# Kernel tuning notes

Measured on AMD Instinct MI355X. Metric: run time of the kernel, lower is better.

The kernel has to match this reference:

```python
import jax, jax.numpy as jnp
import numpy as np
import itertools

DIM_X, DIM_Y = 3, 3
MAX_DIGIT = DIM_X * DIM_Y          # 9
NUM_NODES = MAX_DIGIT ** 2         # 81
EMBED = 16
HID = 96
BATCH = 256
ITERS = 4


def determine_edges(dim_x, dim_y):
    md = dim_x * dim_y
    rows = []
    for r in range(md):
        for c in range(md):
            s = {(r, i) for i in range(md)} | {(i, c) for i in range(md)}
            xm, ym = r // dim_x * dim_x, c // dim_y * dim_y
            s |= set(itertools.product(range(xm, xm + dim_x), range(ym, ym + dim_y)))
            s -= {(r, c)}
            rows.append(sorted(i * md + j for i, j in s))
    return np.asarray(rows, dtype=np.int32)  # [81, 20]


def mlp3(x, w0, b0, w1, b1, w2, b2):
    # MLP([a,b,c,d]): two ReLU hidden layers, linear output
    x = jax.nn.relu(x @ w0.T + b0)
    x = jax.nn.relu(x @ w1.T + b1)
    return x @ w2.T + b2


def setup_inputs() -> dict:
    key = jax.random.key(0)
    keys = iter(jax.random.split(key, 40))

    def lin(din, dout):
        kw, kb = jax.random.split(next(keys))
        lim = 1.0 / np.sqrt(din)
        w = jax.random.uniform(kw, (dout, din), jnp.float32, -lim, lim)
        b = jax.random.uniform(kb, (dout,), jnp.float32, -lim, lim)
        return w, b

    embed = jax.random.normal(next(keys), (MAX_DIGIT + 1, EMBED), jnp.float32)

    in_w0, in_b0 = lin(EMBED, HID); in_w1, in_b1 = lin(HID, HID); in_w2, in_b2 = lin(HID, HID)
    f_w0, f_b0 = lin(2 * HID, HID); f_w1, f_b1 = lin(HID, HID); f_w2, f_b2 = lin(HID, HID)
    g_w0, g_b0 = lin(2 * HID, HID); g_w1, g_b1 = lin(HID, HID); g_w2, g_b2 = lin(HID, HID)
    r_w0, r_b0 = lin(HID, HID); r_w1, r_b1 = lin(HID, HID); r_w2, r_b2 = lin(HID, MAX_DIGIT)

    lim = 1.0 / np.sqrt(HID)
    lstm_wih = jax.random.uniform(next(keys), (4 * HID, HID), jnp.float32, -lim, lim)
    lstm_whh = jax.random.uniform(next(keys), (4 * HID, HID), jnp.float32, -lim, lim)
    lstm_bih = jax.random.uniform(next(keys), (4 * HID,), jnp.float32, -lim, lim)
    lstm_bhh = jax.random.uniform(next(keys), (4 * HID,), jnp.float32, -lim, lim)

    grids = jax.random.randint(next(keys), (BATCH, NUM_NODES), 0, MAX_DIGIT + 1)
    c0 = jax.random.normal(next(keys), (BATCH * NUM_NODES, HID), jnp.float32)
    edges = jnp.asarray(determine_edges(DIM_X, DIM_Y))

    return dict(embed=embed,
                in_w0=in_w0, in_b0=in_b0, in_w1=in_w1, in_b1=in_b1, in_w2=in_w2, in_b2=in_b2,
                f_w0=f_w0, f_b0=f_b0, f_w1=f_w1, f_b1=f_b1, f_w2=f_w2, f_b2=f_b2,
                g_w0=g_w0, g_b0=g_b0, g_w1=g_w1, g_b1=g_b1, g_w2=g_w2, g_b2=g_b2,
                lstm_wih=lstm_wih, lstm_whh=lstm_whh, lstm_bih=lstm_bih, lstm_bhh=lstm_bhh,
                r_w0=r_w0, r_b0=r_b0, r_w1=r_w1, r_b1=r_b1, r_w2=r_w2, r_b2=r_b2,
                c0=c0, grids=grids, edges=edges, iters=ITERS)


def reference(embed,
              in_w0, in_b0, in_w1, in_b1, in_w2, in_b2,
              f_w0, f_b0, f_w1, f_b1, f_w2, f_b2,
              g_w0, g_b0, g_w1, g_b1, g_w2, g_b2,
              lstm_wih, lstm_whh, lstm_bih, lstm_bhh,
              r_w0, r_b0, r_w1, r_b1, r_w2, r_b2,
              c0, grids, edges, iters):
    B, N = grids.shape
    K = edges.shape[1]
    emb = embed[grids]                                   # [B, N, EMBED]
    X = mlp3(emb, in_w0, in_b0, in_w1, in_b1, in_w2, in_b2)  # [B, N, HID]
    H = X
    h = X.reshape(B * N, HID)
    c = c0
    outputs = []
    for _ in range(iters):
        # gather neighbor states: [B, N, K, HID]
        Hn = H[:, edges]
        Hs = jnp.broadcast_to(H[:, :, None, :], Hn.shape)
        pair = jnp.concatenate([Hs, Hn], axis=-1)        # [B, N, K, 2*HID]
        M = mlp3(pair, f_w0, f_b0, f_w1, f_b1, f_w2, f_b2).sum(axis=2)  # [B, N, HID]
        gin = mlp3(jnp.concatenate([X, M], axis=-1),
                   g_w0, g_b0, g_w1, g_b1, g_w2, g_b2).reshape(B * N, HID)
        # single-step LSTM (torch gate order: i, f, g, o)
        gates = gin @ lstm_wih.T + lstm_bih + h @ lstm_whh.T + lstm_bhh
        gi, gf, gg, go = jnp.split(gates, 4, axis=-1)
        c = jax.nn.sigmoid(gf) * c + jax.nn.sigmoid(gi) * jnp.tanh(gg)
        h = jax.nn.sigmoid(go) * jnp.tanh(c)
        H = h.reshape(B, N, HID)
        outputs.append(mlp3(H, r_w0, r_b0, r_w1, r_b1, r_w2, r_b2))  # [B, N, MAX_DIGIT]
    return jnp.stack(outputs)  # [iters, B, N, MAX_DIGIT]
```

## Files before the change

kernel.cpp:

```cpp
#include <hip/hip_runtime.h>
#include <hip/hip_bf16.h>

typedef __hip_bfloat16 bf16;
typedef __attribute__((ext_vector_type(8))) short short8;
typedef __attribute__((ext_vector_type(8))) __bf16 bf16x8;
typedef __attribute__((ext_vector_type(4))) float f32x4;

#define BN 20736
#define NNODE 81
#define KNB 20

__device__ inline float bf2f(short s) {
  union { unsigned u; float f; } x; x.u = ((unsigned)(unsigned short)s) << 16; return x.f;
}
__device__ inline short f2bf(float f) {
  __hip_bfloat16 h = __float2bfloat16(f);
  return *reinterpret_cast<short*>(&h);
}
__device__ inline bf16x8 ld8(const bf16* p) {
  return __builtin_bit_cast(bf16x8, *(const short8*)p);
}

__device__ inline void zacc3(f32x4 acc[3]) {
  #pragma unroll
  for (int nt = 0; nt < 3; ++nt) acc[nt] = (f32x4){0.f, 0.f, 0.f, 0.f};
}
__device__ inline void load_w48(const bf16* __restrict__ W, int ldw, int n0, int lr, int lq,
                                bf16x8 wf[3][3]) {
  #pragma unroll
  for (int nt = 0; nt < 3; ++nt)
    #pragma unroll
    for (int ks = 0; ks < 3; ++ks)
      wf[nt][ks] = ld8(&W[(size_t)(n0 + nt * 16 + lr) * ldw + ks * 32 + lq * 8]);
}
__device__ inline void gemm48(const bf16x8 af[3], const bf16x8 wf[3][3], f32x4 acc[3]) {
  #pragma unroll
  for (int ks = 0; ks < 3; ++ks)
    #pragma unroll
    for (int nt = 0; nt < 3; ++nt)
      acc[nt] = __builtin_amdgcn_mfma_f32_16x16x32_bf16(af[ks], wf[nt][ks], acc[nt], 0, 0, 0);
}
__device__ inline void acc_store_cs(float* xw, const f32x4 acc[3], int lr, int lq, int n0) {
  #pragma unroll
  for (int nt = 0; nt < 3; ++nt)
    #pragma unroll
    for (int r = 0; r < 4; ++r)
      xw[(lq * 4 + r) * 100 + n0 + nt * 16 + lr] = acc[nt][r];
}
__device__ inline void xbuf_frag(const float* xw, int lr, int lq,
                                 const float* __restrict__ bias, float bscale,
                                 const bf16* residRow, int act,
                                 bf16x8 af[3]) {
  #pragma unroll
  for (int ks = 0; ks < 3; ++ks) {
    const int c0 = ks * 32 + lq * 8;
    float4 x0 = *(const float4*)&xw[lr * 100 + c0];
    float4 x1 = *(const float4*)&xw[lr * 100 + c0 + 4];
    float xv[8] = {x0.x, x0.y, x0.z, x0.w, x1.x, x1.y, x1.z, x1.w};
    if (bias) {
      float4 b0 = *(const float4*)&bias[c0];
      float4 b1 = *(const float4*)&bias[c0 + 4];
      float bv[8] = {b0.x, b0.y, b0.z, b0.w, b1.x, b1.y, b1.z, b1.w};
      #pragma unroll
      for (int j = 0; j < 8; ++j) xv[j] += bscale * bv[j];
    }
    if (residRow) {
      short8 r8 = *(const short8*)&residRow[c0];
      #pragma unroll
      for (int j = 0; j < 8; ++j) xv[j] += bf2f(r8[j]);
    }
    short8 o;
    #pragma unroll
    for (int j = 0; j < 8; ++j) {
      float v = xv[j];
      if (act) v = fmaxf(v, 0.f);
      o[j] = f2bf(v);
    }
    af[ks] = __builtin_bit_cast(bf16x8, o);
  }
}
__device__ inline void store_frag(bf16* dst, int lq, const bf16x8 af[3]) {
  #pragma unroll
  for (int ks = 0; ks < 3; ++ks)
    *(short8*)&dst[ks * 32 + lq * 8] = __builtin_bit_cast(short8, af[ks]);
}

__global__ __launch_bounds__(256) void prep_k(
    const float* in_w1, const float* in_w2, const float* f_w1, const float* f_w2,
    const float* g_w1, const float* g_w2, const float* r_w0, const float* r_w1,
    const float* r_w2, const float* wih, const float* whh, const float* g_w0,
    const float* f_w0, const float* in_w0, const float* f_b0,
    bf16* inw1b, bf16* inw2b, bf16* fw1b, bf16* fw2b,
    bf16* gw1b, bf16* gw2b, bf16* rw0b, bf16* rw1b,
    bf16* rw2b, bf16* wihb, bf16* whhb, bf16* gw0b,
    bf16* wfnb, bf16* w0pb, float* bias_fn)
{
  int idx = blockIdx.x * 256 + threadIdx.x;
  int y = blockIdx.y;
  const float* src = nullptr; bf16* dst = nullptr; int cnt = 0;
  switch (y) {
    case 0:  src = in_w1; dst = inw1b; cnt = 9216;  break;
    case 1:  src = in_w2; dst = inw2b; cnt = 9216;  break;
    case 2:  src = f_w1;  dst = fw1b;  cnt = 9216;  break;
    case 3:  src = f_w2;  dst = fw2b;  cnt = 9216;  break;
    case 4:  src = g_w1;  dst = gw1b;  cnt = 9216;  break;
    case 5:  src = g_w2;  dst = gw2b;  cnt = 9216;  break;
    case 6:  src = r_w0;  dst = rw0b;  cnt = 9216;  break;
    case 7:  src = r_w1;  dst = rw1b;  cnt = 9216;  break;
    case 8:  src = r_w2;  dst = rw2b;  cnt = 864;   break;
    case 9:  src = wih;   dst = wihb;  cnt = 36864; break;
    case 10: src = whh;   dst = whhb;  cnt = 36864; break;
    case 11: src = g_w0;  dst = gw0b;  cnt = 18432; break;
    case 12: {
      if (idx < 18432) {
        int n = idx / 96, k = idx - n * 96;
        float v = (n < 96) ? f_w0[n * 192 + k] : f_w0[(n - 96) * 192 + 96 + k];
        wfnb[idx] = __float2bfloat16(v);
      }
      return;
    }
    case 13: {
      if (idx < 3072) {
        int n = idx >> 5, k = idx & 31;
        w0pb[idx] = __float2bfloat16(k < 16 ? in_w0[n * 16 + k] : 0.f);
      }
      return;
    }
    default: {
      if (idx < 192) bias_fn[idx] = (idx < 96) ? f_b0[idx] : 0.f;
      return;
    }
  }
  if (idx < cnt) dst[idx] = __float2bfloat16(src[idx]);
}

__global__ __launch_bounds__(256) void embed_k(const float* __restrict__ embed,
                                               const int* __restrict__ grids,
                                               bf16* __restrict__ emb) {
  int idx = blockIdx.x * 256 + threadIdx.x;
  if (idx >= BN * 32) return;
  int r = idx >> 5, k = idx & 31;
  emb[idx] = __float2bfloat16(k < 16 ? embed[grids[r] * 16 + k] : 0.f);
}

__global__ __launch_bounds__(256) void fused_in_k(
    const bf16* __restrict__ emb, const bf16* __restrict__ w0pb, const float* __restrict__ in_b0,
    const bf16* __restrict__ inw1b, const float* __restrict__ in_b1,
    const bf16* __restrict__ inw2b, const float* __restrict__ in_b2,
    const bf16* __restrict__ gw0b, const float* __restrict__ g_b0,
    const bf16* __restrict__ wfnb, const float* __restrict__ bias_fn,
    bf16* __restrict__ X, bf16* __restrict__ Xg, bf16* __restrict__ P)
{
  __shared__ float xbuf[2][2][1600];
  const int t = threadIdx.x, w = t >> 6, lane = t & 63, lr = lane & 15, lq = lane >> 4;
  const int mh = w >> 1, ch = w & 1, n0 = ch * 48;
  const int m0 = blockIdx.x * 32 + mh * 16;
  float* x0 = xbuf[0][mh];
  float* x1 = xbuf[1][mh];
  bf16x8 wf[3][3]; f32x4 acc[3]; bf16x8 af[3];

  bf16x8 a0 = ld8(&emb[(size_t)(m0 + lr) * 32 + lq * 8]);
  #pragma unroll
  for (int nt = 0; nt < 3; ++nt)
    wf[nt][0] = ld8(&w0pb[(size_t)(n0 + nt * 16 + lr) * 32 + lq * 8]);
  zacc3(acc);
  #pragma unroll
  for (int nt = 0; nt < 3; ++nt)
    acc[nt] = __builtin_amdgcn_mfma_f32_16x16x32_bf16(a0, wf[nt][0], acc[nt], 0, 0, 0);
  acc_store_cs(x0, acc, lr, lq, n0);
  __syncthreads();
  xbuf_frag(x0, lr, lq, in_b0, 1.f, nullptr, 1, af);
  load_w48(inw1b, 96, n0, lr, lq, wf); zacc3(acc); gemm48(af, wf, acc);
  acc_store_cs(x1, acc, lr, lq, n0);
  __syncthreads();
  xbuf_frag(x1, lr, lq, in_b1, 1.f, nullptr, 1, af);
  load_w48(inw2b, 96, n0, lr, lq, wf); zacc3(acc); gemm48(af, wf, acc);
  acc_store_cs(x0, acc, lr, lq, n0);
  __syncthreads();
  bf16x8 xf[3];
  xbuf_frag(x0, lr, lq, in_b2, 1.f, nullptr, 0, xf);
  if (ch == 0) store_frag(&X[(size_t)(m0 + lr) * 96], lq, xf);
  load_w48(gw0b, 192, n0, lr, lq, wf); zacc3(acc); gemm48(xf, wf, acc);
  acc_store_cs(x1, acc, lr, lq, n0);
  __syncthreads();
  xbuf_frag(x1, lr, lq, g_b0, 1.f, nullptr, 0, af);
  if (ch == 0) store_frag(&Xg[(size_t)(m0 + lr) * 96], lq, af);
  #pragma unroll
  for (int ph = 0; ph < 2; ++ph) {
    float* xb = ph ? x1 : x0;
    load_w48(wfnb + (size_t)ph * 96 * 96, 96, n0, lr, lq, wf); zacc3(acc); gemm48(xf, wf, acc);
    acc_store_cs(xb, acc, lr, lq, n0);
    __syncthreads();
    xbuf_frag(xb, lr, lq, bias_fn + ph * 96, 1.f, nullptr, 0, af);
    if (ch == 0) store_frag(&P[(size_t)(m0 + lr) * 192 + ph * 96], lq, af);
  }
}

__global__ __launch_bounds__(256) void edge_k(
    const bf16* __restrict__ P, const bf16* __restrict__ w1bf,
    const float* __restrict__ b1, const int* __restrict__ edges,
    const bf16* __restrict__ fw2b, const float* __restrict__ f_b2,
    bf16* __restrict__ M)
{
  __shared__ short zs[160 * 104];
  __shared__ short sbuf[16 * 104];
  const int t = threadIdx.x;
  const int swz = (blockIdx.x & 7) * 324 + (blockIdx.x >> 3);
  const int ng0 = swz * 2;
  const int w = t >> 6, lane = t & 63, lr = lane & 15, lq = lane >> 4;
  const int g = w >> 1, ch = w & 1, n0 = ch * 48, zb = g * 80;

  bf16x8 wf[3][3];
  #pragma unroll
  for (int nt = 0; nt < 3; ++nt)
    #pragma unroll
    for (int ks = 0; ks < 3; ++ks)
      wf[nt][ks] = ld8(&w1bf[(size_t)(n0 + nt * 16 + lr) * 96 + ks * 32 + lq * 8]);

  for (int i = t; i < 8 * 104; i += 256) sbuf[(8 + i / 104) * 104 + (i % 104)] = 0;
  for (int cc = t; cc < 160 * 12; cc += 256) {
    int zrow = cc / 12, c8 = cc - zrow * 12;
    int gg = zrow >= 80 ? 1 : 0;
    int row = zrow - gg * 80;
    int p = row / 20, j = row - p * 20;
    int gr = (ng0 + gg) * 4 + p;
    int b = gr / NNODE, i = gr - b * NNODE;
    int e = edges[i * KNB + j];
    short8 a8 = *(const short8*)&P[(size_t)gr * 192 + c8 * 8];
    short8 n8 = *(const short8*)&P[((size_t)b * NNODE + e) * 192 + 96 + c8 * 8];
    short8 z;
    #pragma unroll
    for (int q = 0; q < 8; ++q)
      z[q] = f2bf(fmaxf(bf2f(a8[q]) + bf2f(n8[q]), 0.f));
    *(short8*)&zs[zrow * 104 + c8 * 8] = z;
  }
  __syncthreads();

  f32x4 acc[5][3];
  #pragma unroll
  for (int mt = 0; mt < 5; ++mt)
    #pragma unroll
    for (int nt = 0; nt < 3; ++nt) acc[mt][nt] = (f32x4){0.f, 0.f, 0.f, 0.f};

  #pragma unroll
  for (int ks = 0; ks < 3; ++ks) {
    const int koff = ks * 32 + lq * 8;
    #pragma unroll
    for (int mt = 0; mt < 5; ++mt) {
      bf16x8 af = __builtin_bit_cast(bf16x8, *(const short8*)&zs[(zb + mt * 16 + lr) * 104 + koff]);
      #pragma unroll
      for (int nt = 0; nt < 3; ++nt)
        acc[mt][nt] = __builtin_amdgcn_mfma_f32_16x16x32_bf16(af, wf[nt][ks], acc[mt][nt], 0, 0, 0);
    }
  }

  float bv[3];
  #pragma unroll
  for (int nt = 0; nt < 3; ++nt) bv[nt] = b1[n0 + nt * 16 + lr];
  float nodeacc[4][3];
  #pragma unroll
  for (int pp = 0; pp < 4; ++pp)
    #pragma unroll
    for (int nt = 0; nt < 3; ++nt) nodeacc[pp][nt] = 0.f;
  #pragma unroll
  for (int mt = 0; mt < 5; ++mt)
    #pragma unroll
    for (int nt = 0; nt < 3; ++nt)
      #pragma unroll
      for (int r = 0; r < 4; ++r) {
        int row = mt * 16 + lq * 4 + r;
        int p = row / 20;
        float v = fmaxf(acc[mt][nt][r] + bv[nt], 0.f);
        #pragma unroll
        for (int pp = 0; pp < 4; ++pp)
          nodeacc[pp][nt] += (p == pp) ? v : 0.f;
      }
  #pragma unroll
  for (int pp = 0; pp < 4; ++pp)
    #pragma unroll
    for (int nt = 0; nt < 3; ++nt) {
      float v = nodeacc[pp][nt];
      v += __shfl_xor(v, 16, 64);
      v += __shfl_xor(v, 32, 64);
      if (lq == 0)
        sbuf[(g * 4 + pp) * 104 + n0 + nt * 16 + lr] = f2bf(v);
    }
  __syncthreads();
  if (w < 2) {
    const int mn0 = w * 48;
    bf16x8 mwf[3][3];
    #pragma unroll
    for (int nt = 0; nt < 3; ++nt)
      #pragma unroll
      for (int ks = 0; ks < 3; ++ks)
        mwf[nt][ks] = ld8(&fw2b[(size_t)(mn0 + nt * 16 + lr) * 96 + ks * 32 + lq * 8]);
    f32x4 macc[3];
    zacc3(macc);
    #pragma unroll
    for (int ks = 0; ks < 3; ++ks) {
      bf16x8 af = __builtin_bit_cast(bf16x8, *(const short8*)&sbuf[lr * 104 + ks * 32 + lq * 8]);
      #pragma unroll
      for (int nt = 0; nt < 3; ++nt)
        macc[nt] = __builtin_amdgcn_mfma_f32_16x16x32_bf16(af, mwf[nt][ks], macc[nt], 0, 0, 0);
    }
    #pragma unroll
    for (int nt = 0; nt < 3; ++nt) {
      int col = mn0 + nt * 16 + lr;
      float bb = (float)KNB * f_b2[col];
      #pragma unroll
      for (int r = 0; r < 4; ++r) {
        int row = lq * 4 + r;
        if (row < 8)
          M[(size_t)(ng0 * 4 + row) * 96 + col] = __float2bfloat16(macc[nt][r] + bb);
      }
    }
  }
}

__global__ __launch_bounds__(128) void fused_iter_k(
    const bf16* __restrict__ Min,
    const bf16* __restrict__ gw0b, const bf16* __restrict__ Xg,
    const bf16* __restrict__ gw1b, const float* __restrict__ g_b1,
    const bf16* __restrict__ gw2b, const float* __restrict__ g_b2,
    const bf16* __restrict__ Hin,
    const bf16* __restrict__ wihb, const bf16* __restrict__ whhb,
    const float* __restrict__ bih, const float* __restrict__ bhh,
    float* __restrict__ c, bf16* __restrict__ Hout,
    const bf16* __restrict__ wfnb, const float* __restrict__ bias_fn, bf16* __restrict__ P,
    const bf16* __restrict__ rw0b, const float* __restrict__ r_b0,
    const bf16* __restrict__ rw1b, const float* __restrict__ r_b1,
    const bf16* __restrict__ rw2b, const float* __restrict__ r_b2,
    float* __restrict__ outp, int doP)
{
  __shared__ float xb0[1600], xb1[1600];
  const int t = threadIdx.x, w = t >> 6, lane = t & 63, lr = lane & 15, lq = lane >> 4;
  const int n0 = w * 48;
  const int m0 = blockIdx.x * 16;

  bf16x8 wfA[3][3], wfB[3][3], af[3];
  f32x4 acc[3];

  #pragma unroll
  for (int ks = 0; ks < 3; ++ks)
    af[ks] = ld8(&Min[(size_t)(m0 + lr) * 96 + ks * 32 + lq * 8]);
  bf16x8 hin[3];
  #pragma unroll
  for (int ks = 0; ks < 3; ++ks)
    hin[ks] = ld8(&Hin[(size_t)(m0 + lr) * 96 + ks * 32 + lq * 8]);

  load_w48(gw0b + 96, 192, n0, lr, lq, wfA);
  zacc3(acc); gemm48(af, wfA, acc);
  load_w48(gw1b, 96, n0, lr, lq, wfB);
  acc_store_cs(xb0, acc, lr, lq, n0);
  __syncthreads();
  xbuf_frag(xb0, lr, lq, nullptr, 0.f, &Xg[(size_t)(m0 + lr) * 96], 1, af);
  zacc3(acc); gemm48(af, wfB, acc);
  load_w48(gw2b, 96, n0, lr, lq, wfA);
  acc_store_cs(xb1, acc, lr, lq, n0);
  __syncthreads();
  xbuf_frag(xb1, lr, lq, g_b1, 1.f, nullptr, 1, af);
  zacc3(acc); gemm48(af, wfA, acc);
  acc_store_cs(xb0, acc, lr, lq, n0);
  __syncthreads();
  bf16x8 gf[3];
  xbuf_frag(xb0, lr, lq, g_b2, 1.f, nullptr, 0, gf);

  float cv[3][4];
  #pragma unroll
  for (int nt = 0; nt < 3; ++nt)
    #pragma unroll
    for (int r = 0; r < 4; ++r)
      cv[nt][r] = c[(size_t)(m0 + lq * 4 + r) * 96 + n0 + nt * 16 + lr];

  f32x4 ga[4][3];
  #pragma unroll
  for (int g4 = 0; g4 < 4; ++g4)
    #pragma unroll
    for (int nt = 0; nt < 3; ++nt) ga[g4][nt] = (f32x4){0.f, 0.f, 0.f, 0.f};
  #pragma unroll
  for (int g4 = 0; g4 < 4; ++g4)
    #pragma unroll
    for (int nt = 0; nt < 3; ++nt) {
      size_t nrow = (size_t)(g4 * 96 + n0 + nt * 16 + lr) * 96;
      #pragma unroll
      for (int ks = 0; ks < 3; ++ks) {
        ga[g4][nt] = __builtin_amdgcn_mfma_f32_16x16x32_bf16(
            gf[ks], ld8(&wihb[nrow + ks * 32 + lq * 8]), ga[g4][nt], 0, 0, 0);
        ga[g4][nt] = __builtin_amdgcn_mfma_f32_16x16x32_bf16(
            hin[ks], ld8(&whhb[nrow + ks * 32 + lq * 8]), ga[g4][nt], 0, 0, 0);
      }
    }
  #pragma unroll
  for (int nt = 0; nt < 3; ++nt) {
    int col = n0 + nt * 16 + lr;
    float bvi = bih[col] + bhh[col];
    float bvf = bih[96 + col] + bhh[96 + col];
    float bvg = bih[192 + col] + bhh[192 + col];
    float bvo = bih[288 + col] + bhh[288 + col];
    #pragma unroll
    for (int r = 0; r < 4; ++r) {
      int m = m0 + lq * 4 + r;
      size_t idx = (size_t)m * 96 + col;
      float gi = ga[0][nt][r] + bvi;
      float gfv = ga[1][nt][r] + bvf;
      float gg = ga[2][nt][r] + bvg;
      float go = ga[3][nt][r] + bvo;
      float si = 1.f / (1.f + expf(-gi));
      float sf = 1.f / (1.f + expf(-gfv));
      float so = 1.f / (1.f + expf(-go));
      float tg = tanhf(gg);
      float cn = sf * cv[nt][r] + si * tg;
      if (doP) c[idx] = cn;
      xb1[(lq * 4 + r) * 100 + col] = so * tanhf(cn);
    }
  }
  __syncthreads();
  bf16x8 hf[3];
  xbuf_frag(xb1, lr, lq, nullptr, 0.f, nullptr, 0, hf);

  if (doP) {
    for (int cc = t; cc < 192; cc += 128) {
      int row = cc / 12, c8 = cc - row * 12;
      short8 o;
      #pragma unroll
      for (int j = 0; j < 8; ++j) o[j] = f2bf(xb1[row * 100 + c8 * 8 + j]);
      *(short8*)&Hout[(size_t)(m0 + row) * 96 + c8 * 8] = o;
    }
    load_w48(wfnb, 96, n0, lr, lq, wfA);
    zacc3(acc); gemm48(hf, wfA, acc);
    load_w48(wfnb + 96 * 96, 96, n0, lr, lq, wfB);
    #pragma unroll
    for (int nt = 0; nt < 3; ++nt) {
      float bvv = bias_fn[n0 + nt * 16 + lr];
      #pragma unroll
      for (int r = 0; r < 4; ++r)
        xb0[(lq * 4 + r) * 100 + n0 + nt * 16 + lr] = acc[nt][r] + bvv;
    }
    __syncthreads();
    for (int cc = t; cc < 192; cc += 128) {
      int row = cc / 12, c8 = cc - row * 12;
      short8 o;
      #pragma unroll
      for (int j = 0; j < 8; ++j) o[j] = f2bf(xb0[row * 100 + c8 * 8 + j]);
      *(short8*)&P[(size_t)(m0 + row) * 192 + c8 * 8] = o;
    }
    zacc3(acc); gemm48(hf, wfB, acc);
    #pragma unroll
    for (int nt = 0; nt < 3; ++nt) {
      float bvv = bias_fn[96 + n0 + nt * 16 + lr];
      #pragma unroll
      for (int r = 0; r < 4; ++r)
        xb1[(lq * 4 + r) * 100 + n0 + nt * 16 + lr] = acc[nt][r] + bvv;
    }
    __syncthreads();
    for (int cc = t; cc < 192; cc += 128) {
      int row = cc / 12, c8 = cc - row * 12;
      short8 o;
      #pragma unroll
      for (int j = 0; j < 8; ++j) o[j] = f2bf(xb1[row * 100 + c8 * 8 + j]);
      *(short8*)&P[(size_t)(m0 + row) * 192 + 96 + c8 * 8] = o;
    }
  }

  load_w48(rw0b, 96, n0, lr, lq, wfA);
  zacc3(acc); gemm48(hf, wfA, acc);
  load_w48(rw1b, 96, n0, lr, lq, wfB);
  __syncthreads();
  acc_store_cs(xb0, acc, lr, lq, n0);
  __syncthreads();
  xbuf_frag(xb0, lr, lq, r_b0, 1.f, nullptr, 1, af);
  zacc3(acc); gemm48(af, wfB, acc);
  acc_store_cs(xb1, acc, lr, lq, n0);
  __syncthreads();
  xbuf_frag(xb1, lr, lq, r_b1, 1.f, nullptr, 1, af);
  if (w == 0) {
    bf16x8 w9[3];
    #pragma unroll
    for (int ks = 0; ks < 3; ++ks) {
      short8 s = {0, 0, 0, 0, 0, 0, 0, 0};
      if (lr < 9) s = *(const short8*)&rw2b[(size_t)lr * 96 + ks * 32 + lq * 8];
      w9[ks] = __builtin_bit_cast(bf16x8, s);
    }
    f32x4 a9 = (f32x4){0.f, 0.f, 0.f, 0.f};
    #pragma unroll
    for (int ks = 0; ks < 3; ++ks)
      a9 = __builtin_amdgcn_mfma_f32_16x16x32_bf16(af[ks], w9[ks], a9, 0, 0, 0);
    if (lr < 9) {
      float bb = r_b2[lr];
      #pragma unroll
      for (int r = 0; r < 4; ++r)
        outp[(size_t)(m0 + lq * 4 + r) * 9 + lr] = a9[r] + bb;
    }
  }
}

extern "C" void kernel_launch(void* const* d_in, const int* in_sizes, int n_in,
                              void* d_out, int out_size, void* d_ws, size_t ws_size,
                              hipStream_t stream) {
  const float* embed   = (const float*)d_in[0];
  const float* in_w0   = (const float*)d_in[1];
  const float* in_b0   = (const float*)d_in[2];
  const float* in_w1   = (const float*)d_in[3];
  const float* in_b1   = (const float*)d_in[4];
  const float* in_w2   = (const float*)d_in[5];
  const float* in_b2   = (const float*)d_in[6];
  const float* f_w0    = (const float*)d_in[7];
  const float* f_b0    = (const float*)d_in[8];
  const float* f_w1    = (const float*)d_in[9];
  const float* f_b1    = (const float*)d_in[10];
  const float* f_w2    = (const float*)d_in[11];
  const float* f_b2    = (const float*)d_in[12];
  const float* g_w0    = (const float*)d_in[13];
  const float* g_b0    = (const float*)d_in[14];
  const float* g_w1    = (const float*)d_in[15];
  const float* g_b1    = (const float*)d_in[16];
  const float* g_w2    = (const float*)d_in[17];
  const float* g_b2    = (const float*)d_in[18];
  const float* wih     = (const float*)d_in[19];
  const float* whh     = (const float*)d_in[20];
  const float* bih     = (const float*)d_in[21];
  const float* bhh     = (const float*)d_in[22];
  const float* r_w0    = (const float*)d_in[23];
  const float* r_b0    = (const float*)d_in[24];
  const float* r_w1    = (const float*)d_in[25];
  const float* r_b1    = (const float*)d_in[26];
  const float* r_w2    = (const float*)d_in[27];
  const float* r_b2    = (const float*)d_in[28];
  const float* c0      = (const float*)d_in[29];
  const int*   grids   = (const int*)d_in[30];
  const int*   edges   = (const int*)d_in[31];

  float* out = (float*)d_out;
  const int iters = out_size / (BN * 9);

  float* c    = (float*)d_ws;
  bf16* H0    = (bf16*)(c + (size_t)BN * 96);
  bf16* H1    = H0 + (size_t)BN * 96;
  bf16* Xg    = H1 + (size_t)BN * 96;
  bf16* P     = Xg + (size_t)BN * 96;
  bf16* Mb    = P  + (size_t)BN * 192;
  bf16* emb   = Mb + (size_t)BN * 96;
  bf16* w0pb  = emb + (size_t)BN * 32;
  bf16* wfnb  = w0pb + 3072;
  bf16* inw1b = wfnb + 18432;
  bf16* inw2b = inw1b + 9216;
  bf16* fw1b  = inw2b + 9216;
  bf16* fw2b  = fw1b + 9216;
  bf16* gw0b  = fw2b + 9216;
  bf16* gw1b  = gw0b + 18432;
  bf16* gw2b  = gw1b + 9216;
  bf16* rw0b  = gw2b + 9216;
  bf16* rw1b  = rw0b + 9216;
  bf16* rw2b  = rw1b + 9216;
  bf16* wihb  = rw2b + 864;
  bf16* whhb  = wihb + 36864;
  float* bias_fn = (float*)(whhb + 36864);

  prep_k<<<dim3(144, 15), 256, 0, stream>>>(
      in_w1, in_w2, f_w1, f_w2, g_w1, g_w2, r_w0, r_w1, r_w2, wih, whh, g_w0,
      f_w0, in_w0, f_b0,
      inw1b, inw2b, fw1b, fw2b, gw1b, gw2b, rw0b, rw1b, rw2b, wihb, whhb, gw0b,
      wfnb, w0pb, bias_fn);
  embed_k<<<(BN * 32) / 256, 256, 0, stream>>>(embed, grids, emb);
  fused_in_k<<<BN / 32, 256, 0, stream>>>(emb, w0pb, in_b0, inw1b, in_b1, inw2b, in_b2,
                                          gw0b, g_b0, wfnb, bias_fn, H0, Xg, P);
  hipMemcpyAsync(c, c0, (size_t)BN * 96 * sizeof(float), hipMemcpyDeviceToDevice, stream);

  for (int it = 0; it < iters; ++it) {
    bf16* Hin  = (it & 1) ? H1 : H0;
    bf16* Hout = (it & 1) ? H0 : H1;
    edge_k<<<BN / 8, 256, 0, stream>>>(P, fw1b, f_b1, edges, fw2b, f_b2, Mb);
    fused_iter_k<<<BN / 16, 128, 0, stream>>>(
        Mb, gw0b, Xg, gw1b, g_b1, gw2b, g_b2,
        Hin, wihb, whhb, bih, bhh, c, Hout,
        wfnb, bias_fn, P, rw0b, r_b0, rw1b, r_b1, rw2b, r_b2,
        out + (size_t)it * BN * 9, it < iters - 1 ? 1 : 0);
  }
}
```

Baseline: 331.6 us.

## Fuse edge message kernel into per-iteration node update kernel

```diff
diff --git a/kernel.cpp b/kernel.cpp
--- a/kernel.cpp
+++ b/kernel.cpp
@@ -196,129 +196,11 @@
   }
 }
 
-__global__ __launch_bounds__(256) void edge_k(
-    const bf16* __restrict__ P, const bf16* __restrict__ w1bf,
-    const float* __restrict__ b1, const int* __restrict__ edges,
+__global__ __launch_bounds__(256) void iter_k(
+    const bf16* __restrict__ Pin, bf16* __restrict__ Pout,
+    const bf16* __restrict__ fw1b, const float* __restrict__ f_b1,
+    const int* __restrict__ edges,
     const bf16* __restrict__ fw2b, const float* __restrict__ f_b2,
-    bf16* __restrict__ M)
-{
-  __shared__ short zs[160 * 104];
-  __shared__ short sbuf[16 * 104];
-  const int t = threadIdx.x;
-  const int swz = (blockIdx.x & 7) * 324 + (blockIdx.x >> 3);
-  const int ng0 = swz * 2;
-  const int w = t >> 6, lane = t & 63, lr = lane & 15, lq = lane >> 4;
-  const int g = w >> 1, ch = w & 1, n0 = ch * 48, zb = g * 80;
-
-  bf16x8 wf[3][3];
-  #pragma unroll
-  for (int nt = 0; nt < 3; ++nt)
-    #pragma unroll
-    for (int ks = 0; ks < 3; ++ks)
-      wf[nt][ks] = ld8(&w1bf[(size_t)(n0 + nt * 16 + lr) * 96 + ks * 32 + lq * 8]);
-
-  for (int i = t; i < 8 * 104; i += 256) sbuf[(8 + i / 104) * 104 + (i % 104)] = 0;
-  for (int cc = t; cc < 160 * 12; cc += 256) {
-    int zrow = cc / 12, c8 = cc - zrow * 12;
-    int gg = zrow >= 80 ? 1 : 0;
-    int row = zrow - gg * 80;
-    int p = row / 20, j = row - p * 20;
-    int gr = (ng0 + gg) * 4 + p;
-    int b = gr / NNODE, i = gr - b * NNODE;
-    int e = edges[i * KNB + j];
-    short8 a8 = *(const short8*)&P[(size_t)gr * 192 + c8 * 8];
-    short8 n8 = *(const short8*)&P[((size_t)b * NNODE + e) * 192 + 96 + c8 * 8];
-    short8 z;
-    #pragma unroll
-    for (int q = 0; q < 8; ++q)
-      z[q] = f2bf(fmaxf(bf2f(a8[q]) + bf2f(n8[q]), 0.f));
-    *(short8*)&zs[zrow * 104 + c8 * 8] = z;
-  }
-  __syncthreads();
-
-  f32x4 acc[5][3];
-  #pragma unroll
-  for (int mt = 0; mt < 5; ++mt)
-    #pragma unroll
-    for (int nt = 0; nt < 3; ++nt) acc[mt][nt] = (f32x4){0.f, 0.f, 0.f, 0.f};
-
-  #pragma unroll
-  for (int ks = 0; ks < 3; ++ks) {
-    const int koff = ks * 32 + lq * 8;
-    #pragma unroll
-    for (int mt = 0; mt < 5; ++mt) {
-      bf16x8 af = __builtin_bit_cast(bf16x8, *(const short8*)&zs[(zb + mt * 16 + lr) * 104 + koff]);
-      #pragma unroll
-      for (int nt = 0; nt < 3; ++nt)
-        acc[mt][nt] = __builtin_amdgcn_mfma_f32_16x16x32_bf16(af, wf[nt][ks], acc[mt][nt], 0, 0, 0);
-    }
-  }
-
-  float bv[3];
-  #pragma unroll
-  for (int nt = 0; nt < 3; ++nt) bv[nt] = b1[n0 + nt * 16 + lr];
-  float nodeacc[4][3];
-  #pragma unroll
-  for (int pp = 0; pp < 4; ++pp)
-    #pragma unroll
-    for (int nt = 0; nt < 3; ++nt) nodeacc[pp][nt] = 0.f;
-  #pragma unroll
-  for (int mt = 0; mt < 5; ++mt)
-    #pragma unroll
-    for (int nt = 0; nt < 3; ++nt)
-      #pragma unroll
-      for (int r = 0; r < 4; ++r) {
-        int row = mt * 16 + lq * 4 + r;
-        int p = row / 20;
-        float v = fmaxf(acc[mt][nt][r] + bv[nt], 0.f);
-        #pragma unroll
-        for (int pp = 0; pp < 4; ++pp)
-          nodeacc[pp][nt] += (p == pp) ? v : 0.f;
-      }
-  #pragma unroll
-  for (int pp = 0; pp < 4; ++pp)
-    #pragma unroll
-    for (int nt = 0; nt < 3; ++nt) {
-      float v = nodeacc[pp][nt];
-      v += __shfl_xor(v, 16, 64);
-      v += __shfl_xor(v, 32, 64);
-      if (lq == 0)
-        sbuf[(g * 4 + pp) * 104 + n0 + nt * 16 + lr] = f2bf(v);
-    }
-  __syncthreads();
-  if (w < 2) {
-    const int mn0 = w * 48;
-    bf16x8 mwf[3][3];
-    #pragma unroll
-    for (int nt = 0; nt < 3; ++nt)
-      #pragma unroll
-      for (int ks = 0; ks < 3; ++ks)
-        mwf[nt][ks] = ld8(&fw2b[(size_t)(mn0 + nt * 16 + lr) * 96 + ks * 32 + lq * 8]);
-    f32x4 macc[3];
-    zacc3(macc);
-    #pragma unroll
-    for (int ks = 0; ks < 3; ++ks) {
-      bf16x8 af = __builtin_bit_cast(bf16x8, *(const short8*)&sbuf[lr * 104 + ks * 32 + lq * 8]);
-      #pragma unroll
-      for (int nt = 0; nt < 3; ++nt)
-        macc[nt] = __builtin_amdgcn_mfma_f32_16x16x32_bf16(af, mwf[nt][ks], macc[nt], 0, 0, 0);
-    }
-    #pragma unroll
-    for (int nt = 0; nt < 3; ++nt) {
-      int col = mn0 + nt * 16 + lr;
-      float bb = (float)KNB * f_b2[col];
-      #pragma unroll
-      for (int r = 0; r < 4; ++r) {
-        int row = lq * 4 + r;
-        if (row < 8)
-          M[(size_t)(ng0 * 4 + row) * 96 + col] = __float2bfloat16(macc[nt][r] + bb);
-      }
-    }
-  }
-}
-
-__global__ __launch_bounds__(128) void fused_iter_k(
-    const bf16* __restrict__ Min,
     const bf16* __restrict__ gw0b, const bf16* __restrict__ Xg,
     const bf16* __restrict__ gw1b, const float* __restrict__ g_b1,
     const bf16* __restrict__ gw2b, const float* __restrict__ g_b2,
@@ -326,44 +208,136 @@
     const bf16* __restrict__ wihb, const bf16* __restrict__ whhb,
     const float* __restrict__ bih, const float* __restrict__ bhh,
     float* __restrict__ c, bf16* __restrict__ Hout,
-    const bf16* __restrict__ wfnb, const float* __restrict__ bias_fn, bf16* __restrict__ P,
+    const bf16* __restrict__ wfnb, const float* __restrict__ bias_fn,
     const bf16* __restrict__ rw0b, const float* __restrict__ r_b0,
     const bf16* __restrict__ rw1b, const float* __restrict__ r_b1,
     const bf16* __restrict__ rw2b, const float* __restrict__ r_b2,
     float* __restrict__ outp, int doP)
 {
-  __shared__ float xb0[1600], xb1[1600];
+  __shared__ __align__(16) char ldsA[160 * 104 * 2];
+  __shared__ __align__(16) char ldsB[32 * 104 * 2];
+  short* zs   = (short*)ldsA;
+  float* xbuf = (float*)ldsA;
+  short* sbuf = (short*)ldsB;
+
   const int t = threadIdx.x, w = t >> 6, lane = t & 63, lr = lane & 15, lq = lane >> 4;
-  const int n0 = w * 48;
-  const int m0 = blockIdx.x * 16;
-
+  const int swz = (blockIdx.x & 7) * 81 + (blockIdx.x >> 3);
+  const int m0blk = swz * 32;
+  const int g = w >> 1, ch = w & 1, n0 = ch * 48;
+
+  bf16x8 wf1[3][3];
+  #pragma unroll
+  for (int nt = 0; nt < 3; ++nt)
+    #pragma unroll
+    for (int ks = 0; ks < 3; ++ks)
+      wf1[nt][ks] = ld8(&fw1b[(size_t)(n0 + nt * 16 + lr) * 96 + ks * 32 + lq * 8]);
+  float b1v[3];
+  #pragma unroll
+  for (int nt = 0; nt < 3; ++nt) b1v[nt] = f_b1[n0 + nt * 16 + lr];
+
+  #pragma unroll 1
+  for (int rep = 0; rep < 4; ++rep) {
+    for (int cc = t; cc < 160 * 12; cc += 256) {
+      int zrow = cc / 12, c8 = cc - zrow * 12;
+      int gg = zrow >= 80 ? 1 : 0;
+      int row = zrow - gg * 80;
+      int p = row / 20, j = row - p * 20;
+      int gr = m0blk + (rep * 2 + gg) * 4 + p;
+      int b = gr / NNODE, i = gr - b * NNODE;
+      int e = edges[i * KNB + j];
+      short8 a8 = *(const short8*)&Pin[(size_t)gr * 192 + c8 * 8];
+      short8 n8 = *(const short8*)&Pin[((size_t)b * NNODE + e) * 192 + 96 + c8 * 8];
+      short8 z;
+      #pragma unroll
+      for (int q = 0; q < 8; ++q)
+        z[q] = f2bf(fmaxf(bf2f(a8[q]) + bf2f(n8[q]), 0.f));
+      *(short8*)&zs[zrow * 104 + c8 * 8] = z;
+    }
+    __syncthreads();
+
+    const int zb = g * 80;
+    f32x4 eacc[5][3];
+    #pragma unroll
+    for (int mt = 0; mt < 5; ++mt)
+      #pragma unroll
+      for (int nt = 0; nt < 3; ++nt) eacc[mt][nt] = (f32x4){0.f, 0.f, 0.f, 0.f};
+    #pragma unroll
+    for (int ks = 0; ks < 3; ++ks) {
+      const int koff = ks * 32 + lq * 8;
+      #pragma unroll
+      for (int mt = 0; mt < 5; ++mt) {
+        bf16x8 af = __builtin_bit_cast(bf16x8, *(const short8*)&zs[(zb + mt * 16 + lr) * 104 + koff]);
+        #pragma unroll
+        for (int nt = 0; nt < 3; ++nt)
+          eacc[mt][nt] = __builtin_amdgcn_mfma_f32_16x16x32_bf16(af, wf1[nt][ks], eacc[mt][nt], 0, 0, 0);
+      }
+    }
+    float na[4][3];
+    #pragma unroll
+    for (int pp = 0; pp < 4; ++pp)
+      #pragma unroll
+      for (int nt = 0; nt < 3; ++nt) na[pp][nt] = 0.f;
+    #pragma unroll
+    for (int mt = 0; mt < 5; ++mt)
+      #pragma unroll
+      for (int nt = 0; nt < 3; ++nt)
+        #pragma unroll
+        for (int r = 0; r < 4; ++r) {
+          int row = mt * 16 + lq * 4 + r;
+          int p = row / 20;
+          float v = fmaxf(eacc[mt][nt][r] + b1v[nt], 0.f);
+          #pragma unroll
+          for (int pp = 0; pp < 4; ++pp) na[pp][nt] += (p == pp) ? v : 0.f;
+        }
+    #pragma unroll
+    for (int pp = 0; pp < 4; ++pp)
+      #pragma unroll
+      for (int nt = 0; nt < 3; ++nt) {
+        float v = na[pp][nt];
+        v += __shfl_xor(v, 16, 64);
+        v += __shfl_xor(v, 32, 64);
+        if (lq == 0)
+          sbuf[(rep * 8 + g * 4 + pp) * 104 + n0 + nt * 16 + lr] = f2bf(v);
+      }
+    __syncthreads();
+  }
+
+  const int mh = w >> 1;
+  const int m0 = m0blk + mh * 16;
+  float* x0 = xbuf + (0 * 2 + mh) * 1600;
+  float* x1 = xbuf + (1 * 2 + mh) * 1600;
   bf16x8 wfA[3][3], wfB[3][3], af[3];
   f32x4 acc[3];
 
-  #pragma unroll
-  for (int ks = 0; ks < 3; ++ks)
-    af[ks] = ld8(&Min[(size_t)(m0 + lr) * 96 + ks * 32 + lq * 8]);
   bf16x8 hin[3];
   #pragma unroll
   for (int ks = 0; ks < 3; ++ks)
     hin[ks] = ld8(&Hin[(size_t)(m0 + lr) * 96 + ks * 32 + lq * 8]);
 
-  load_w48(gw0b + 96, 192, n0, lr, lq, wfA);
+  #pragma unroll
+  for (int ks = 0; ks < 3; ++ks)
+    af[ks] = ld8((const bf16*)&sbuf[(mh * 16 + lr) * 104 + ks * 32 + lq * 8]);
+  load_w48(fw2b, 96, n0, lr, lq, wfA);
   zacc3(acc); gemm48(af, wfA, acc);
-  load_w48(gw1b, 96, n0, lr, lq, wfB);
-  acc_store_cs(xb0, acc, lr, lq, n0);
-  __syncthreads();
-  xbuf_frag(xb0, lr, lq, nullptr, 0.f, &Xg[(size_t)(m0 + lr) * 96], 1, af);
+  load_w48(gw0b + 96, 192, n0, lr, lq, wfB);
+  acc_store_cs(x0, acc, lr, lq, n0);
+  __syncthreads();
+  xbuf_frag(x0, lr, lq, f_b2, (float)KNB, nullptr, 0, af);
   zacc3(acc); gemm48(af, wfB, acc);
-  load_w48(gw2b, 96, n0, lr, lq, wfA);
-  acc_store_cs(xb1, acc, lr, lq, n0);
-  __syncthreads();
-  xbuf_frag(xb1, lr, lq, g_b1, 1.f, nullptr, 1, af);
+  load_w48(gw1b, 96, n0, lr, lq, wfA);
+  acc_store_cs(x1, acc, lr, lq, n0);
+  __syncthreads();
+  xbuf_frag(x1, lr, lq, nullptr, 0.f, &Xg[(size_t)(m0 + lr) * 96], 1, af);
   zacc3(acc); gemm48(af, wfA, acc);
-  acc_store_cs(xb0, acc, lr, lq, n0);
+  load_w48(gw2b, 96, n0, lr, lq, wfB);
+  acc_store_cs(x0, acc, lr, lq, n0);
+  __syncthreads();
+  xbuf_frag(x0, lr, lq, g_b1, 1.f, nullptr, 1, af);
+  zacc3(acc); gemm48(af, wfB, acc);
+  acc_store_cs(x1, acc, lr, lq, n0);
   __syncthreads();
   bf16x8 gf[3];
-  xbuf_frag(xb0, lr, lq, g_b2, 1.f, nullptr, 0, gf);
+  xbuf_frag(x1, lr, lq, g_b2, 1.f, nullptr, 0, gf);
 
   float cv[3][4];
   #pragma unroll
@@ -411,20 +385,21 @@
       float tg = tanhf(gg);
       float cn = sf * cv[nt][r] + si * tg;
       if (doP) c[idx] = cn;
-      xb1[(lq * 4 + r) * 100 + col] = so * tanhf(cn);
+      x1[(lq * 4 + r) * 100 + col] = so * tanhf(cn);
     }
   }
   __syncthreads();
   bf16x8 hf[3];
-  xbuf_frag(xb1, lr, lq, nullptr, 0.f, nullptr, 0, hf);
+  xbuf_frag(x1, lr, lq, nullptr, 0.f, nullptr, 0, hf);
 
   if (doP) {
-    for (int cc = t; cc < 192; cc += 128) {
+    for (int cc = t; cc < 384; cc += 256) {
       int row = cc / 12, c8 = cc - row * 12;
+      const float* xs = xbuf + (1 * 2 + (row >> 4)) * 1600;
       short8 o;
       #pragma unroll
-      for (int j = 0; j < 8; ++j) o[j] = f2bf(xb1[row * 100 + c8 * 8 + j]);
-      *(short8*)&Hout[(size_t)(m0 + row) * 96 + c8 * 8] = o;
+      for (int j = 0; j < 8; ++j) o[j] = f2bf(xs[(row & 15) * 100 + c8 * 8 + j]);
+      *(short8*)&Hout[(size_t)(m0blk + row) * 96 + c8 * 8] = o;
     }
     load_w48(wfnb, 96, n0, lr, lq, wfA);
     zacc3(acc); gemm48(hf, wfA, acc);
@@ -434,31 +409,34 @@
       float bvv = bias_fn[n0 + nt * 16 + lr];
       #pragma unroll
       for (int r = 0; r < 4; ++r)
-        xb0[(lq * 4 + r) * 100 + n0 + nt * 16 + lr] = acc[nt][r] + bvv;
+        x0[(lq * 4 + r) * 100 + n0 + nt * 16 + lr] = acc[nt][r] + bvv;
     }
     __syncthreads();
-    for (int cc = t; cc < 192; cc += 128) {
+    for (int cc = t; cc < 384; cc += 256) {
       int row = cc / 12, c8 = cc - row * 12;
+      const float* xs = xbuf + (0 * 2 + (row >> 4)) * 1600;
       short8 o;
       #pragma unroll
-      for (int j = 0; j < 8; ++j) o[j] = f2bf(xb0[row * 100 + c8 * 8 + j]);
-      *(short8*)&P[(size_t)(m0 + row) * 192 + c8 * 8] = o;
+      for (int j = 0; j < 8; ++j) o[j] = f2bf(xs[(row & 15) * 100 + c8 * 8 + j]);
+      *(short8*)&Pout[(size_t)(m0blk + row) * 192 + c8 * 8] = o;
     }
     zacc3(acc); gemm48(hf, wfB, acc);
+    __syncthreads();
     #pragma unroll
     for (int nt = 0; nt < 3; ++nt) {
       float bvv = bias_fn[96 + n0 + nt * 16 + lr];
       #pragma unroll
       for (int r = 0; r < 4; ++r)
-        xb1[(lq * 4 + r) * 100 + n0 + nt * 16 + lr] = acc[nt][r] + bvv;
+        x1[(lq * 4 + r) * 100 + n0 + nt * 16 + lr] = acc[nt][r] + bvv;
     }
     __syncthreads();
-    for (int cc = t; cc < 192; cc += 128) {
+    for (int cc = t; cc < 384; cc += 256) {
       int row = cc / 12, c8 = cc - row * 12;
+      const float* xs = xbuf + (1 * 2 + (row >> 4)) * 1600;
       short8 o;
       #pragma unroll
-      for (int j = 0; j < 8; ++j) o[j] = f2bf(xb1[row * 100 + c8 * 8 + j]);
-      *(short8*)&P[(size_t)(m0 + row) * 192 + 96 + c8 * 8] = o;
+      for (int j = 0; j < 8; ++j) o[j] = f2bf(xs[(row & 15) * 100 + c8 * 8 + j]);
+      *(short8*)&Pout[(size_t)(m0blk + row) * 192 + 96 + c8 * 8] = o;
     }
   }
 
@@ -466,14 +444,14 @@
   zacc3(acc); gemm48(hf, wfA, acc);
   load_w48(rw1b, 96, n0, lr, lq, wfB);
   __syncthreads();
-  acc_store_cs(xb0, acc, lr, lq, n0);
-  __syncthreads();
-  xbuf_frag(xb0, lr, lq, r_b0, 1.f, nullptr, 1, af);
+  acc_store_cs(x0, acc, lr, lq, n0);
+  __syncthreads();
+  xbuf_frag(x0, lr, lq, r_b0, 1.f, nullptr, 1, af);
   zacc3(acc); gemm48(af, wfB, acc);
-  acc_store_cs(xb1, acc, lr, lq, n0);
-  __syncthreads();
-  xbuf_frag(xb1, lr, lq, r_b1, 1.f, nullptr, 1, af);
-  if (w == 0) {
+  acc_store_cs(x1, acc, lr, lq, n0);
+  __syncthreads();
+  xbuf_frag(x1, lr, lq, r_b1, 1.f, nullptr, 1, af);
+  if (ch == 0) {
     bf16x8 w9[3];
     #pragma unroll
     for (int ks = 0; ks < 3; ++ks) {
@@ -537,9 +515,9 @@
   bf16* H0    = (bf16*)(c + (size_t)BN * 96);
   bf16* H1    = H0 + (size_t)BN * 96;
   bf16* Xg    = H1 + (size_t)BN * 96;
-  bf16* P     = Xg + (size_t)BN * 96;
-  bf16* Mb    = P  + (size_t)BN * 192;
-  bf16* emb   = Mb + (size_t)BN * 96;
+  bf16* P0    = Xg + (size_t)BN * 96;
+  bf16* P1    = P0 + (size_t)BN * 192;
+  bf16* emb   = P1 + (size_t)BN * 192;
   bf16* w0pb  = emb + (size_t)BN * 32;
   bf16* wfnb  = w0pb + 3072;
   bf16* inw1b = wfnb + 18432;
@@ -563,17 +541,20 @@
       wfnb, w0pb, bias_fn);
   embed_k<<<(BN * 32) / 256, 256, 0, stream>>>(embed, grids, emb);
   fused_in_k<<<BN / 32, 256, 0, stream>>>(emb, w0pb, in_b0, inw1b, in_b1, inw2b, in_b2,
-                                          gw0b, g_b0, wfnb, bias_fn, H0, Xg, P);
+                                          gw0b, g_b0, wfnb, bias_fn, H0, Xg, P0);
   hipMemcpyAsync(c, c0, (size_t)BN * 96 * sizeof(float), hipMemcpyDeviceToDevice, stream);
 
+  bf16* Pcur = P0;
+  bf16* Pnxt = P1;
   for (int it = 0; it < iters; ++it) {
     bf16* Hin  = (it & 1) ? H1 : H0;
     bf16* Hout = (it & 1) ? H0 : H1;
-    edge_k<<<BN / 8, 256, 0, stream>>>(P, fw1b, f_b1, edges, fw2b, f_b2, Mb);
-    fused_iter_k<<<BN / 16, 128, 0, stream>>>(
-        Mb, gw0b, Xg, gw1b, g_b1, gw2b, g_b2,
+    iter_k<<<BN / 32, 256, 0, stream>>>(
+        Pcur, Pnxt, fw1b, f_b1, edges, fw2b, f_b2,
+        gw0b, Xg, gw1b, g_b1, gw2b, g_b2,
         Hin, wihb, whhb, bih, bhh, c, Hout,
-        wfnb, bias_fn, P, rw0b, r_b0, rw1b, r_b1, rw2b, r_b2,
+        wfnb, bias_fn, rw0b, r_b0, rw1b, r_b1, rw2b, r_b2,
         out + (size_t)it * BN * 9, it < iters - 1 ? 1 : 0);
-  }
-}
+    bf16* tmp = Pcur; Pcur = Pnxt; Pnxt = tmp;
+  }
+}
```

Result: slower. 396.2 us (+19.5%).

## Fuse embedding gather into input MLP and shrink edge kernel blocks

Applied to the files above, without the earlier changes.

```diff
diff --git a/kernel.cpp b/kernel.cpp
--- a/kernel.cpp
+++ b/kernel.cpp
@@ -134,17 +134,9 @@
   if (idx < cnt) dst[idx] = __float2bfloat16(src[idx]);
 }
 
-__global__ __launch_bounds__(256) void embed_k(const float* __restrict__ embed,
-                                               const int* __restrict__ grids,
-                                               bf16* __restrict__ emb) {
-  int idx = blockIdx.x * 256 + threadIdx.x;
-  if (idx >= BN * 32) return;
-  int r = idx >> 5, k = idx & 31;
-  emb[idx] = __float2bfloat16(k < 16 ? embed[grids[r] * 16 + k] : 0.f);
-}
-
 __global__ __launch_bounds__(256) void fused_in_k(
-    const bf16* __restrict__ emb, const bf16* __restrict__ w0pb, const float* __restrict__ in_b0,
+    const float* __restrict__ embed, const int* __restrict__ grids,
+    const bf16* __restrict__ w0pb, const float* __restrict__ in_b0,
     const bf16* __restrict__ inw1b, const float* __restrict__ in_b1,
     const bf16* __restrict__ inw2b, const float* __restrict__ in_b2,
     const bf16* __restrict__ gw0b, const float* __restrict__ g_b0,
@@ -159,7 +151,15 @@
   float* x1 = xbuf[1][mh];
   bf16x8 wf[3][3]; f32x4 acc[3]; bf16x8 af[3];
 
-  bf16x8 a0 = ld8(&emb[(size_t)(m0 + lr) * 32 + lq * 8]);
+  short8 es = {0, 0, 0, 0, 0, 0, 0, 0};
+  if (lq < 2) {
+    int gidx = grids[m0 + lr];
+    float4 e0 = *(const float4*)&embed[gidx * 16 + lq * 8];
+    float4 e1 = *(const float4*)&embed[gidx * 16 + lq * 8 + 4];
+    es[0] = f2bf(e0.x); es[1] = f2bf(e0.y); es[2] = f2bf(e0.z); es[3] = f2bf(e0.w);
+    es[4] = f2bf(e1.x); es[5] = f2bf(e1.y); es[6] = f2bf(e1.z); es[7] = f2bf(e1.w);
+  }
+  bf16x8 a0 = __builtin_bit_cast(bf16x8, es);
   #pragma unroll
   for (int nt = 0; nt < 3; ++nt)
     wf[nt][0] = ld8(&w0pb[(size_t)(n0 + nt * 16 + lr) * 32 + lq * 8]);
@@ -196,34 +196,34 @@
   }
 }
 
-__global__ __launch_bounds__(256) void edge_k(
+__global__ __launch_bounds__(128) void edge_k(
     const bf16* __restrict__ P, const bf16* __restrict__ w1bf,
     const float* __restrict__ b1, const int* __restrict__ edges,
     const bf16* __restrict__ fw2b, const float* __restrict__ f_b2,
     bf16* __restrict__ M)
 {
-  __shared__ short zs[160 * 104];
+  __shared__ short zs[80 * 104];
   __shared__ short sbuf[16 * 104];
   const int t = threadIdx.x;
-  const int swz = (blockIdx.x & 7) * 324 + (blockIdx.x >> 3);
-  const int ng0 = swz * 2;
+  const int grp = (blockIdx.x & 7) * 648 + (blockIdx.x >> 3);
   const int w = t >> 6, lane = t & 63, lr = lane & 15, lq = lane >> 4;
-  const int g = w >> 1, ch = w & 1, n0 = ch * 48, zb = g * 80;
-
-  bf16x8 wf[3][3];
+  const int n0 = w * 48;
+
+  bf16x8 wf1[3][3];
   #pragma unroll
   for (int nt = 0; nt < 3; ++nt)
     #pragma unroll
     for (int ks = 0; ks < 3; ++ks)
-      wf[nt][ks] = ld8(&w1bf[(size_t)(n0 + nt * 16 + lr) * 96 + ks * 32 + lq * 8]);
-
-  for (int i = t; i < 8 * 104; i += 256) sbuf[(8 + i / 104) * 104 + (i % 104)] = 0;
-  for (int cc = t; cc < 160 * 12; cc += 256) {
-    int zrow = cc / 12, c8 = cc - zrow * 12;
-    int gg = zrow >= 80 ? 1 : 0;
-    int row = zrow - gg * 80;
+      wf1[nt][ks] = ld8(&w1bf[(size_t)(n0 + nt * 16 + lr) * 96 + ks * 32 + lq * 8]);
+  float b1v[3];
+  #pragma unroll
+  for (int nt = 0; nt < 3; ++nt) b1v[nt] = b1[n0 + nt * 16 + lr];
+
+  for (int i = t; i < 12 * 104; i += 128) sbuf[(4 + i / 104) * 104 + (i % 104)] = 0;
+  for (int cc = t; cc < 80 * 12; cc += 128) {
+    int row = cc / 12, c8 = cc - row * 12;
     int p = row / 20, j = row - p * 20;
-    int gr = (ng0 + gg) * 4 + p;
+    int gr = grp * 4 + p;
     int b = gr / NNODE, i = gr - b * NNODE;
     int e = edges[i * KNB + j];
     short8 a8 = *(const short8*)&P[(size_t)gr * 192 + c8 * 8];
@@ -232,7 +232,7 @@
     #pragma unroll
     for (int q = 0; q < 8; ++q)
       z[q] = f2bf(fmaxf(bf2f(a8[q]) + bf2f(n8[q]), 0.f));
-    *(short8*)&zs[zrow * 104 + c8 * 8] = z;
+    *(short8*)&zs[row * 104 + c8 * 8] = z;
   }
   __syncthreads();
 
@@ -241,22 +241,18 @@
   for (int mt = 0; mt < 5; ++mt)
     #pragma unroll
     for (int nt = 0; nt < 3; ++nt) acc[mt][nt] = (f32x4){0.f, 0.f, 0.f, 0.f};
-
   #pragma unroll
   for (int ks = 0; ks < 3; ++ks) {
     const int koff = ks * 32 + lq * 8;
     #pragma unroll
     for (int mt = 0; mt < 5; ++mt) {
-      bf16x8 af = __builtin_bit_cast(bf16x8, *(const short8*)&zs[(zb + mt * 16 + lr) * 104 + koff]);
+      bf16x8 af = __builtin_bit_cast(bf16x8, *(const short8*)&zs[(mt * 16 + lr) * 104 + koff]);
       #pragma unroll
       for (int nt = 0; nt < 3; ++nt)
-        acc[mt][nt] = __builtin_amdgcn_mfma_f32_16x16x32_bf16(af, wf[nt][ks], acc[mt][nt], 0, 0, 0);
-    }
-  }
-
-  float bv[3];
-  #pragma unroll
-  for (int nt = 0; nt < 3; ++nt) bv[nt] = b1[n0 + nt * 16 + lr];
+        acc[mt][nt] = __builtin_amdgcn_mfma_f32_16x16x32_bf16(af, wf1[nt][ks], acc[mt][nt], 0, 0, 0);
+    }
+  }
+
   float nodeacc[4][3];
   #pragma unroll
   for (int pp = 0; pp < 4; ++pp)
@@ -270,7 +266,7 @@
       for (int r = 0; r < 4; ++r) {
         int row = mt * 16 + lq * 4 + r;
         int p = row / 20;
-        float v = fmaxf(acc[mt][nt][r] + bv[nt], 0.f);
+        float v = fmaxf(acc[mt][nt][r] + b1v[nt], 0.f);
         #pragma unroll
         for (int pp = 0; pp < 4; ++pp)
           nodeacc[pp][nt] += (p == pp) ? v : 0.f;
@@ -283,36 +279,33 @@
       v += __shfl_xor(v, 16, 64);
       v += __shfl_xor(v, 32, 64);
       if (lq == 0)
-        sbuf[(g * 4 + pp) * 104 + n0 + nt * 16 + lr] = f2bf(v);
-    }
-  __syncthreads();
-  if (w < 2) {
-    const int mn0 = w * 48;
-    bf16x8 mwf[3][3];
+        sbuf[pp * 104 + n0 + nt * 16 + lr] = f2bf(v);
+    }
+  __syncthreads();
+
+  bf16x8 mwf[3][3];
+  #pragma unroll
+  for (int nt = 0; nt < 3; ++nt)
+    #pragma unroll
+    for (int ks = 0; ks < 3; ++ks)
+      mwf[nt][ks] = ld8(&fw2b[(size_t)(n0 + nt * 16 + lr) * 96 + ks * 32 + lq * 8]);
+  f32x4 macc[3];
+  zacc3(macc);
+  #pragma unroll
+  for (int ks = 0; ks < 3; ++ks) {
+    bf16x8 af = __builtin_bit_cast(bf16x8, *(const short8*)&sbuf[lr * 104 + ks * 32 + lq * 8]);
     #pragma unroll
     for (int nt = 0; nt < 3; ++nt)
-      #pragma unroll
-      for (int ks = 0; ks < 3; ++ks)
-        mwf[nt][ks] = ld8(&fw2b[(size_t)(mn0 + nt * 16 + lr) * 96 + ks * 32 + lq * 8]);
-    f32x4 macc[3];
-    zacc3(macc);
-    #pragma unroll
-    for (int ks = 0; ks < 3; ++ks) {
-      bf16x8 af = __builtin_bit_cast(bf16x8, *(const short8*)&sbuf[lr * 104 + ks * 32 + lq * 8]);
-      #pragma unroll
-      for (int nt = 0; nt < 3; ++nt)
-        macc[nt] = __builtin_amdgcn_mfma_f32_16x16x32_bf16(af, mwf[nt][ks], macc[nt], 0, 0, 0);
-    }
+      macc[nt] = __builtin_amdgcn_mfma_f32_16x16x32_bf16(af, mwf[nt][ks], macc[nt], 0, 0, 0);
+  }
+  if (lq == 0) {
     #pragma unroll
     for (int nt = 0; nt < 3; ++nt) {
-      int col = mn0 + nt * 16 + lr;
+      int col = n0 + nt * 16 + lr;
       float bb = (float)KNB * f_b2[col];
       #pragma unroll
-      for (int r = 0; r < 4; ++r) {
-        int row = lq * 4 + r;
-        if (row < 8)
-          M[(size_t)(ng0 * 4 + row) * 96 + col] = __float2bfloat16(macc[nt][r] + bb);
-      }
+      for (int r = 0; r < 4; ++r)
+        M[(size_t)(grp * 4 + r) * 96 + col] = __float2bfloat16(macc[nt][r] + bb);
     }
   }
 }
@@ -539,8 +532,7 @@
   bf16* Xg    = H1 + (size_t)BN * 96;
   bf16* P     = Xg + (size_t)BN * 96;
   bf16* Mb    = P  + (size_t)BN * 192;
-  bf16* emb   = Mb + (size_t)BN * 96;
-  bf16* w0pb  = emb + (size_t)BN * 32;
+  bf16* w0pb  = Mb + (size_t)BN * 96;
   bf16* wfnb  = w0pb + 3072;
   bf16* inw1b = wfnb + 18432;
   bf16* inw2b = inw1b + 9216;
@@ -561,15 +553,15 @@
       f_w0, in_w0, f_b0,
       inw1b, inw2b, fw1b, fw2b, gw1b, gw2b, rw0b, rw1b, rw2b, wihb, whhb, gw0b,
       wfnb, w0pb, bias_fn);
-  embed_k<<<(BN * 32) / 256, 256, 0, stream>>>(embed, grids, emb);
-  fused_in_k<<<BN / 32, 256, 0, stream>>>(emb, w0pb, in_b0, inw1b, in_b1, inw2b, in_b2,
-                                          gw0b, g_b0, wfnb, bias_fn, H0, Xg, P);
+  fused_in_k<<<BN / 32, 256, 0, stream>>>(embed, grids, w0pb, in_b0, inw1b, in_b1,
+                                          inw2b, in_b2, gw0b, g_b0, wfnb, bias_fn,
+                                          H0, Xg, P);
   hipMemcpyAsync(c, c0, (size_t)BN * 96 * sizeof(float), hipMemcpyDeviceToDevice, stream);
 
   for (int it = 0; it < iters; ++it) {
     bf16* Hin  = (it & 1) ? H1 : H0;
     bf16* Hout = (it & 1) ? H0 : H1;
-    edge_k<<<BN / 8, 256, 0, stream>>>(P, fw1b, f_b1, edges, fw2b, f_b2, Mb);
+    edge_k<<<BN / 4, 128, 0, stream>>>(P, fw1b, f_b1, edges, fw2b, f_b2, Mb);
     fused_iter_k<<<BN / 16, 128, 0, stream>>>(
         Mb, gw0b, Xg, gw1b, g_b1, gw2b, g_b2,
         Hin, wihb, whhb, bih, bhh, c, Hout,
```

After: 327.6 us. Within noise of the previous version (-1.2%).
